# Performance work log

Measured on AMD Instinct MI355X. Metric: run time of the kernel, lower is better.

Reference implementation:

```python
import jax, jax.numpy as jnp
import numpy as np
import math

# normalizer: the module takes it as a callable; we use a standard smooth
# inverse-norm normalizer 1/sqrt(x^2 + eps) applied to the e_inf-like component.
_EPS = 1e-3

def _normalizer(x):
    return 1.0 / jnp.sqrt(x * x + _EPS)


def _dist_vec(tri, basis):
    # tri: (B,H,N,C,5); basis: (5,5,6)
    # vec[...,z] = sum_{x,y} basis[x,y,z] * tri_n[...,x] * tri_n[...,y]
    tri_n = tri * _normalizer(tri[..., 4:5])
    return jnp.einsum('xyz,bhncx,bhncy->bhncz', basis, tri_n, tri_n)


def setup_inputs() -> dict:
    key = jax.random.key(0)
    ks = jax.random.split(key, 8)
    B, H, N, C, S = 1, 8, 4096, 8, 16
    return {
        'q_mv': jax.random.normal(ks[0], (B, H, N, C, 32), jnp.float32),
        'k_mv': jax.random.normal(ks[1], (B, H, N, C, 32), jnp.float32),
        'v_mv': jax.random.normal(ks[2], (B, H, N, C, 32), jnp.float32),
        'q_s': jax.random.normal(ks[3], (B, H, N, S), jnp.float32),
        'k_s': jax.random.normal(ks[4], (B, H, N, S), jnp.float32),
        'v_s': jax.random.normal(ks[5], (B, H, N, S), jnp.float32),
        'basis_q': jax.random.normal(ks[6], (5, 5, 6), jnp.float32),
        'basis_k': jax.random.normal(ks[7], (5, 5, 6), jnp.float32),
    }


def reference(q_mv, k_mv, v_mv, q_s, k_s, v_s, basis_q, basis_k):
    B, H, N, C_qk, _ = q_mv.shape
    C_v = v_mv.shape[-2]
    S_qk = q_s.shape[-1]
    S_v = v_s.shape[-1]
    NUM_IP = 30   # len(_INNER_PRODUCT_WO_EXTREMES_IDX) = indices 1..30
    NUM_DIST = 6
    n_qk = C_qk * (NUM_IP + NUM_DIST) + S_qk
    n_v = C_v * 32 + S_v
    n_ch = 8 * (-(-max(n_qk, n_v) // 8))  # round up to multiple of 8

    # grade-1 components -> distance features
    q_dist = _dist_vec(q_mv[..., 1:6], basis_q)  # (B,H,N,C,6)
    k_dist = _dist_vec(k_mv[..., 1:6], basis_k)

    # inner-product components (indices 1..30)
    q_ip = q_mv[..., 1:31].reshape(B, H, N, C_qk * NUM_IP)
    k_ip = k_mv[..., 1:31].reshape(B, H, N, C_qk * NUM_IP)

    zpad_qk = jnp.zeros((B, H, N, n_ch - n_qk), q_mv.dtype)
    zpad_v = jnp.zeros((B, H, N, n_ch - n_v), v_mv.dtype)

    q = jnp.concatenate([q_ip, q_dist.reshape(B, H, N, -1), q_s, zpad_qk], -1)
    k = jnp.concatenate([k_ip, k_dist.reshape(B, H, N, -1), k_s, zpad_qk], -1)
    v = jnp.concatenate([v_mv.reshape(B, H, N, C_v * 32), v_s, zpad_v], -1)
    k = k * math.sqrt(n_ch / n_qk)

    # standard scaled dot-product attention with scale 1/sqrt(n_ch)
    scale = 1.0 / math.sqrt(n_ch)
    scores = jnp.einsum('bhqd,bhkd->bhqk', q, k) * scale
    attn = jax.nn.softmax(scores, axis=-1)
    v_out = jnp.einsum('bhqk,bhkd->bhqd', attn, v)

    v_out_mv = v_out[..., :C_v * 32].reshape(B, H, N, C_v, 32)
    v_out_s = v_out[..., C_v * 32:C_v * 32 + S_v]
    return (v_out_mv, v_out_s)
```

## Files before the change

### kernel.cpp

```cpp
#include <hip/hip_runtime.h>
#include <math.h>

typedef short bf16x8 __attribute__((ext_vector_type(8)));
typedef float f32x4 __attribute__((ext_vector_type(4)));
typedef int   i32x4 __attribute__((ext_vector_type(4)));

#define HH 8
#define NN 4096
#define DIP 256
#define DDX 256
#define DKM 192
#define DV 272
#define BN 32
#define NT (NN/BN)

typedef const __attribute__((address_space(1))) unsigned int* gp_t;
typedef __attribute__((address_space(3))) unsigned int* lp_t;
__device__ __forceinline__ void gload16(const void* g, void* l) {
    __builtin_amdgcn_global_load_lds((gp_t)g, (lp_t)l, 16, 0, 0);
}

__device__ __forceinline__ unsigned short f2bf(float f) {
    unsigned int u = __float_as_uint(f);
    u = (u + 0x7fffu + ((u >> 16) & 1u)) >> 16;
    return (unsigned short)u;
}
__device__ __forceinline__ float bf2f(unsigned short h) {
    return __uint_as_float(((unsigned int)h) << 16);
}
__device__ __forceinline__ float fexp2(float x) {
    float r;
    asm("v_exp_f32 %0, %1" : "=v"(r) : "v"(x));
    return r;
}
__device__ __forceinline__ signed char q8(float x) {
    int v = __float2int_rn(x * 21.1666667f);
    v = v < -127 ? -127 : (v > 127 ? 127 : v);
    return (signed char)v;
}

#define MFMA16(A,B,C) __builtin_amdgcn_mfma_f32_16x16x32_bf16((A),(B),(C),0,0,0)
#define MFMAI8(A,B,C) __builtin_amdgcn_mfma_i32_16x16x64_i8((A),(B),(C),0,0,0)

__global__ void feat_kernel(const float* __restrict__ mv,
                            const float* __restrict__ sv,
                            const float* __restrict__ basis,
                            float scale, int qmode,
                            signed char* __restrict__ fip,
                            unsigned short* __restrict__ fdx)
{
    __shared__ float sb[150];
    int t = threadIdx.x;
    if (t < 150) sb[t] = basis[t];
    __syncthreads();
    int row = blockIdx.x * 32 + (t >> 3);
    int c = t & 7;
    const float* m = mv + (size_t)row * 256 + c * 32;
    float f[32];
    #pragma unroll
    for (int i = 0; i < 8; ++i) {
        float4 v = ((const float4*)m)[i];
        f[i*4+0] = v.x; f[i*4+1] = v.y; f[i*4+2] = v.z; f[i*4+3] = v.w;
    }
    signed char* ip = fip + (size_t)row * DIP;
    unsigned short* dx = fdx + (size_t)row * (qmode ? DDX : DKM);
    #pragma unroll
    for (int j = 0; j < 30; ++j)
        ip[c*30 + j] = q8(f[1+j]);
    if (c < 2) {
        #pragma unroll
        for (int i = 0; i < 8; ++i)
            ip[240 + c*8 + i] = q8(sv[(size_t)row*16 + c*8 + i]);
    }
    float nn = 1.0f / sqrtf(f[5]*f[5] + 0.001f);
    float tn[5];
    #pragma unroll
    for (int x = 0; x < 5; ++x) tn[x] = f[1+x] * nn;
    #pragma unroll
    for (int z = 0; z < 6; ++z) {
        float acc = 0.f;
        #pragma unroll
        for (int x = 0; x < 5; ++x) {
            #pragma unroll
            for (int y = 0; y < 5; ++y)
                acc = fmaf(sb[(x*5+y)*6 + z] * tn[x], tn[y], acc);
        }
        acc *= scale;
        unsigned short hi = f2bf(acc);
        float r1 = acc - bf2f(hi);
        unsigned short mi = f2bf(r1);
        float r2 = r1 - bf2f(mi);
        unsigned short lo = f2bf(r2);
        int cz = c*6 + z;
        if (qmode) {
            dx[cz]      = hi;  dx[48 + cz]  = hi;
            dx[96 + cz] = mi;  dx[144 + cz] = lo;
            if (cz < 16) { dx[208 + cz] = 0; dx[240 + cz] = 0; }
            if (cz >= 32) { dx[160 + cz] = mi; dx[192 + cz] = hi; }
        } else {
            dx[cz]      = mi;  dx[48 + cz]  = lo;
            dx[96 + cz] = hi;  dx[144 + cz] = hi;
        }
    }
}

__global__ void vtrans_kernel(const float* __restrict__ vmv,
                              const float* __restrict__ vs,
                              unsigned short* __restrict__ dst)
{
    __shared__ unsigned short tile[64][DV];
    int blk = blockIdx.x;
    int h = blk >> 6;
    int n0 = (blk & 63) << 6;
    int t = threadIdx.x;
    #pragma unroll
    for (int it = 0; it < 16; ++it) {
        int v = t + it*256;
        int r = v >> 6;
        int sg = v & 63;
        float4 x = *(const float4*)(vmv + ((size_t)(h*NN + n0 + r))*256 + sg*4);
        tile[r][sg*4+0] = f2bf(x.x);
        tile[r][sg*4+1] = f2bf(x.y);
        tile[r][sg*4+2] = f2bf(x.z);
        tile[r][sg*4+3] = f2bf(x.w);
    }
    #pragma unroll
    for (int it = 0; it < 4; ++it) {
        int v = t + it*256;
        int r = v >> 4;
        int si = v & 15;
        tile[r][256 + si] = f2bf(vs[((size_t)(h*NN + n0 + r))*16 + si]);
    }
    __syncthreads();
    #pragma unroll
    for (int it = 0; it < 17; ++it) {
        int v = t + it*256;
        int dd = v >> 4;
        int sg = v & 15;
        ushort4 o;
        o.x = tile[sg*4+0][dd];
        o.y = tile[sg*4+1][dd];
        o.z = tile[sg*4+2][dd];
        o.w = tile[sg*4+3][dd];
        *(ushort4*)(dst + ((size_t)(h*DV + dd))*NN + n0 + sg*4) = o;
    }
}

__global__ __launch_bounds__(512, 1)
void attn_kernel(const signed char*    __restrict__ Qip,
                 const unsigned short* __restrict__ Qdx,
                 const signed char*    __restrict__ Kip,
                 const unsigned short* __restrict__ Kmx,
                 const unsigned short* __restrict__ Vt,
                 float* __restrict__ out)
{
    __shared__ __align__(128) unsigned short smem[41984];

    int blk = blockIdx.x;
    int sbk = ((blk & 7) << 5) | (blk >> 3);
    int h = sbk >> 5;
    int q0 = (sbk & 31) * 128;
    int tid = threadIdx.x;
    int w = tid >> 6;
    int lane = tid & 63;
    int l15 = lane & 15;
    int l4 = lane >> 4;
    int l7l = l15 & 3;
    int l7h = (l15 >> 2) & 1;
    int x7 = l15 & 7;

    const signed char* qipr = Qip + (size_t)(h*NN + q0 + w*16 + l15) * DIP + l4*16;
    i32x4 qip[4];
    #pragma unroll
    for (int s = 0; s < 4; ++s) qip[s] = *(const i32x4*)(qipr + s*64);
    const unsigned short* qdxr = Qdx + (size_t)(h*NN + q0 + w*16 + l15) * DDX + l4*8;
    bf16x8 qdx[8];
    #pragma unroll
    for (int ks = 0; ks < 8; ++ks) qdx[ks] = *(const bf16x8*)(qdxr + ks*32);

    int cl16 = (l4 ^ l7l) * 16;
    int mA  = l15*384 + cl16 + l7h*64;
    int mB  = l15*384 + cl16 + 64 - l7h*64;
    int vlane = (l15>>1)*128 + (((((l15&1)<<2) | l4) ^ (l15>>1)) << 4);
    int pbR = 75776 + w*1024 + l15*64;
    int pSeg0 = pbR + ((((l4>>1)    ) ^ l7l) << 4) + (l4&1)*8;
    int pSeg1 = pbR + ((((l4>>1) + 2) ^ l7l) << 4) + (l4&1)*8;
    int pRd   = pbR + ((l4 ^ l7l) << 4);
    int kti[4];
    #pragma unroll
    for (int s = 0; s < 4; ++s)
        kti[s] = l15*256 + (((s*4 + l4) ^ x7) << 4);

    int kt8s;
    { int r_ = tid >> 4, sg_ = tid & 15;
      kt8s = r_*256 + ((sg_ ^ (r_ & 7)) << 4); }
    int km0s, km1vt, vt1s, vt2s;
#define KMFL(SLOT, DST) { int r_ = (SLOT)/24, fp_ = (SLOT)%24; \
    int g_ = fp_>>3, po_ = fp_&7; \
    int pl_ = ((((po_>>2)&1) ^ ((r_>>2)&1)) << 2) | ((po_&3) ^ (r_&3)); \
    DST = r_*DKM + (g_*8 + pl_)*8; }
#define VTF(SLOT, DST) { int ch_ = (SLOT) >> 3, ws_ = (SLOT) & 7; int lw_ = ws_ ^ (ch_&7); \
    DST = (ch_*2 + (lw_>>2))*NN + (lw_&3)*8; }
    KMFL(tid, km0s)
    if (tid < 256) { KMFL(tid+512, km1vt) } else { VTF(tid-256, km1vt) }
    VTF(tid+256, vt1s)
    VTF(tid+768, vt2s)
#undef KMFL
#undef VTF

    const signed char*    kiph = Kip + (size_t)h*NN*DIP;
    const unsigned short* kmxh = Kmx + (size_t)h*NN*DKM;
    const unsigned short* vh   = Vt  + (size_t)h*DV*NN;

    f32x4 zero = {0.f, 0.f, 0.f, 0.f};
    i32x4 zi = {0, 0, 0, 0};
    f32x4 oacc[17];
    #pragma unroll
    for (int ct = 0; ct < 17; ++ct) oacc[ct] = zero;
    float mreg = -__builtin_inff();
    float lreg = 0.f;
    const float F = 0.08274443827037988f * (6.0f/127.0f) * (6.0f/127.0f);

#define ISSUE(TILE, BUF) do { \
    const signed char* ks_ = kiph + (size_t)(TILE)*BN*DIP; \
    const unsigned short* ms_ = kmxh + (size_t)(TILE)*BN*DKM; \
    const unsigned short* vs_ = vh + (TILE)*BN; \
    char* ktd_ = (char*)smem + (BUF)*8192; \
    unsigned short* kmd_ = smem + 8192 + (BUF)*6144; \
    unsigned short* vtd_ = smem + 20480 + (BUF)*8704; \
    gload16(ks_ + kt8s, ktd_ + tid*16); \
    gload16(ms_ + km0s, kmd_ + tid*8); \
    if (tid < 256) gload16(ms_ + km1vt, kmd_ + (512+tid)*8); \
    else           gload16(vs_ + km1vt, vtd_ + (tid-256)*8); \
    gload16(vs_ + vt1s, vtd_ + (tid+256)*8); \
    if (tid < 320) gload16(vs_ + vt2s, vtd_ + (tid+768)*8); \
} while (0)

    ISSUE(0, 0);
    int cur = 0;
    #pragma unroll 1
    for (int t = 0; t < NT; ++t) {
        if (t < NT-1) ISSUE(t+1, cur^1);
        if (t < NT-1) {
            if (w < 5) asm volatile("s_waitcnt vmcnt(5)" ::: "memory");
            else       asm volatile("s_waitcnt vmcnt(4)" ::: "memory");
        } else {
            asm volatile("s_waitcnt vmcnt(0)" ::: "memory");
        }
        __builtin_amdgcn_sched_barrier(0);
        __builtin_amdgcn_s_barrier();
        __builtin_amdgcn_sched_barrier(0);

        const char* ktb = (const char*)smem + cur*8192;
        const char* kmb = (const char*)smem + 16384 + cur*12288;
        const char* vtb = (const char*)smem + 40960 + cur*17408;
        f32x4 sacc0 = zero, sacc1 = zero;
        i32x4 si0 = zi, si1 = zi;
        __builtin_amdgcn_s_setprio(1);
        #pragma unroll
        for (int s = 0; s < 4; ++s) {
            i32x4 a0 = *(const i32x4*)(ktb + kti[s]);
            i32x4 a1 = *(const i32x4*)(ktb + 4096 + kti[s]);
            si0 = MFMAI8(a0, qip[s], si0);
            si1 = MFMAI8(a1, qip[s], si1);
        }
        #pragma unroll
        for (int ct = 0; ct < 2; ++ct) {
            const char* kk = kmb + ct*6144;
            bf16x8 ka0 = *(const bf16x8*)(kk + mA);
            bf16x8 ka1 = *(const bf16x8*)(kk + mB);
            bf16x8 ka2 = *(const bf16x8*)(kk + mA + 128);
            bf16x8 kb0 = *(const bf16x8*)(kk + mB + 128);
            bf16x8 kb1 = *(const bf16x8*)(kk + mA + 256);
            bf16x8 kb2 = *(const bf16x8*)(kk + mB + 256);
            f32x4 a = (ct == 0) ? sacc0 : sacc1;
            a = MFMA16(ka0, qdx[0], a);
            a = MFMA16(ka1, qdx[1], a);
            a = MFMA16(ka2, qdx[2], a);
            a = MFMA16(kb0, qdx[3], a);
            a = MFMA16(kb1, qdx[4], a);
            a = MFMA16(kb2, qdx[5], a);
            a = MFMA16(ka0, qdx[3], a);
            a = MFMA16(ka1, qdx[6], a);
            a = MFMA16(kb0, qdx[0], a);
            a = MFMA16(kb1, qdx[7], a);
            if (ct == 0) sacc0 = a; else sacc1 = a;
        }
        __builtin_amdgcn_s_setprio(0);
        f32x4 sn0, sn1;
        sn0[0] = sacc0[0] + F * (float)si0[0];
        sn0[1] = sacc0[1] + F * (float)si0[1];
        sn0[2] = sacc0[2] + F * (float)si0[2];
        sn0[3] = sacc0[3] + F * (float)si0[3];
        sn1[0] = sacc1[0] + F * (float)si1[0];
        sn1[1] = sacc1[1] + F * (float)si1[1];
        sn1[2] = sacc1[2] + F * (float)si1[2];
        sn1[3] = sacc1[3] + F * (float)si1[3];

        float pm = fmaxf(fmaxf(fmaxf(sn0[0], sn0[1]), fmaxf(sn0[2], sn0[3])),
                         fmaxf(fmaxf(sn1[0], sn1[1]), fmaxf(sn1[2], sn1[3])));
        pm = fmaxf(pm, __shfl_xor(pm, 16, 64));
        pm = fmaxf(pm, __shfl_xor(pm, 32, 64));
        if (!__all(pm <= mreg + 8.0f)) {
            float mnew = fmaxf(mreg, pm);
            float al = fexp2(mreg - mnew);
            mreg = mnew;
            lreg *= al;
            float a0 = __shfl(al, l4*4+0, 64);
            float a1 = __shfl(al, l4*4+1, 64);
            float a2 = __shfl(al, l4*4+2, 64);
            float a3 = __shfl(al, l4*4+3, 64);
            #pragma unroll
            for (int ct = 0; ct < 17; ++ct) {
                oacc[ct][0] *= a0; oacc[ct][1] *= a1;
                oacc[ct][2] *= a2; oacc[ct][3] *= a3;
            }
        }
        float p0 = fexp2(sn0[0] - mreg), p1 = fexp2(sn0[1] - mreg);
        float p2 = fexp2(sn0[2] - mreg), p3 = fexp2(sn0[3] - mreg);
        float p4 = fexp2(sn1[0] - mreg), p5 = fexp2(sn1[1] - mreg);
        float p6 = fexp2(sn1[2] - mreg), p7 = fexp2(sn1[3] - mreg);
        lreg += ((p0 + p1) + (p2 + p3)) + ((p4 + p5) + (p6 + p7));
        unsigned r01, r23, r45, r67;
        asm("v_cvt_pk_bf16_f32 %0, %1, %2" : "=v"(r01) : "v"(p0), "v"(p1));
        asm("v_cvt_pk_bf16_f32 %0, %1, %2" : "=v"(r23) : "v"(p2), "v"(p3));
        asm("v_cvt_pk_bf16_f32 %0, %1, %2" : "=v"(r45) : "v"(p4), "v"(p5));
        asm("v_cvt_pk_bf16_f32 %0, %1, %2" : "=v"(r67) : "v"(p6), "v"(p7));
        {
            char* pbp = (char*)smem;
            *(unsigned*)(pbp + pSeg0 + 0) = r01;
            *(unsigned*)(pbp + pSeg0 + 4) = r23;
            *(unsigned*)(pbp + pSeg1 + 0) = r45;
            *(unsigned*)(pbp + pSeg1 + 4) = r67;
        }

        {
            bf16x8 pa = *(const bf16x8*)((const char*)smem + pRd);
            __builtin_amdgcn_s_setprio(1);
            #pragma unroll
            for (int ct = 0; ct < 17; ++ct) {
                bf16x8 bv = *(const bf16x8*)(vtb + vlane + ct*1024);
                oacc[ct] = MFMA16(pa, bv, oacc[ct]);
            }
            __builtin_amdgcn_s_setprio(0);
        }
        __builtin_amdgcn_s_barrier();
        __builtin_amdgcn_sched_barrier(0);
        cur ^= 1;
    }
#undef ISSUE

    float lf = lreg;
    lf += __shfl_xor(lf, 16, 64);
    lf += __shfl_xor(lf, 32, 64);
    const size_t mv_total = (size_t)HH * NN * 256;
    #pragma unroll
    for (int j = 0; j < 4; ++j) {
        float inv = 1.0f / __shfl(lf, l4*4 + j, 64);
        int q = q0 + w*16 + l4*4 + j;
        float* po = out + ((size_t)h*NN + q) * 256 + l15;
        #pragma unroll
        for (int ct = 0; ct < 16; ++ct)
            po[ct*16] = oacc[ct][j] * inv;
        out[mv_total + ((size_t)h*NN + q)*16 + l15] = oacc[16][j] * inv;
    }
}

extern "C" void kernel_launch(void* const* d_in, const int* in_sizes, int n_in,
                              void* d_out, int out_size, void* d_ws, size_t ws_size,
                              hipStream_t stream)
{
    const float* q_mv = (const float*)d_in[0];
    const float* k_mv = (const float*)d_in[1];
    const float* v_mv = (const float*)d_in[2];
    const float* q_s  = (const float*)d_in[3];
    const float* k_s  = (const float*)d_in[4];
    const float* v_s  = (const float*)d_in[5];
    const float* basis_q = (const float*)d_in[6];
    const float* basis_k = (const float*)d_in[7];
    float* out = (float*)d_out;

    signed char* qip8 = (signed char*)d_ws;
    signed char* kip8 = qip8 + (size_t)HH*NN*DIP;
    unsigned short* qdx = (unsigned short*)(kip8 + (size_t)HH*NN*DIP);
    unsigned short* kmx = qdx + (size_t)HH*NN*DDX;
    unsigned short* vt  = kmx + (size_t)HH*NN*DKM;

    const float qscale = 0.08274443827037988f;

    feat_kernel<<<dim3(1024), dim3(256), 0, stream>>>(q_mv, q_s, basis_q, qscale, 1, qip8, qdx);
    feat_kernel<<<dim3(1024), dim3(256), 0, stream>>>(k_mv, k_s, basis_k, 1.0f,   0, kip8, kmx);
    vtrans_kernel<<<dim3(512), dim3(256), 0, stream>>>(v_mv, v_s, vt);
    attn_kernel<<<dim3(256), dim3(512), 0, stream>>>(qip8, qdx, kip8, kmx, vt, out);
}
```

Measured before the change: 280.6 us.

## Double KV tile width and split K/V prefetch into separate pipeline stages

Result: faster. 258.2 us (median of 2 runs) (-8.0%).

```diff
diff --git a/kernel.cpp b/kernel.cpp
--- a/kernel.cpp
+++ b/kernel.cpp
@@ -11,7 +11,7 @@
 #define DDX 256
 #define DKM 192
 #define DV 272
-#define BN 32
+#define BN 64
 #define NT (NN/BN)
 
 typedef const __attribute__((address_space(1))) unsigned int* gp_t;
@@ -154,7 +154,7 @@
                  const unsigned short* __restrict__ Vt,
                  float* __restrict__ out)
 {
-    __shared__ __align__(128) unsigned short smem[41984];
+    __shared__ __align__(128) unsigned short smem[66560];
 
     int blk = blockIdx.x;
     int sbk = ((blk & 7) << 5) | (blk >> 3);
@@ -181,31 +181,34 @@
     int cl16 = (l4 ^ l7l) * 16;
     int mA  = l15*384 + cl16 + l7h*64;
     int mB  = l15*384 + cl16 + 64 - l7h*64;
-    int vlane = (l15>>1)*128 + (((((l15&1)<<2) | l4) ^ (l15>>1)) << 4);
-    int pbR = 75776 + w*1024 + l15*64;
-    int pSeg0 = pbR + ((((l4>>1)    ) ^ l7l) << 4) + (l4&1)*8;
-    int pSeg1 = pbR + ((((l4>>1) + 2) ^ l7l) << 4) + (l4&1)*8;
-    int pRd   = pbR + ((l4 ^ l7l) << 4);
     int kti[4];
     #pragma unroll
     for (int s = 0; s < 4; ++s)
         kti[s] = l15*256 + (((s*4 + l4) ^ x7) << 4);
-
-    int kt8s;
-    { int r_ = tid >> 4, sg_ = tid & 15;
-      kt8s = r_*256 + ((sg_ ^ (r_ & 7)) << 4); }
-    int km0s, km1vt, vt1s, vt2s;
+    int vb0 = (l15>>1)*256 + ((((l15&1)*8 + l4) ^ (l15>>1)) << 4);
+    int vb1 = (l15>>1)*256 + ((((l15&1)*8 + 4 + l4) ^ (l15>>1)) << 4);
+    int pbW = 116736 + w*2048 + l15*128;
+    int pw[4];
+    #pragma unroll
+    for (int kt4 = 0; kt4 < 4; ++kt4)
+        pw[kt4] = pbW + (((kt4*2 + (l4>>1)) ^ x7) << 4) + ((l4&1) << 3);
+    int pr0 = pbW + ((l4 ^ x7) << 4);
+    int pr1 = pbW + (((4+l4) ^ x7) << 4);
+
+    int kts0, kts1;
+    { int idx = tid;       int r_ = idx>>4, sg_ = idx&15; kts0 = r_*256 + ((sg_ ^ (r_&7))<<4); }
+    { int idx = tid+512;   int r_ = idx>>4, sg_ = idx&15; kts1 = r_*256 + ((sg_ ^ (r_&7))<<4); }
+    int kms0, kms1, kms2;
 #define KMFL(SLOT, DST) { int r_ = (SLOT)/24, fp_ = (SLOT)%24; \
     int g_ = fp_>>3, po_ = fp_&7; \
     int pl_ = ((((po_>>2)&1) ^ ((r_>>2)&1)) << 2) | ((po_&3) ^ (r_&3)); \
     DST = r_*DKM + (g_*8 + pl_)*8; }
-#define VTF(SLOT, DST) { int ch_ = (SLOT) >> 3, ws_ = (SLOT) & 7; int lw_ = ws_ ^ (ch_&7); \
-    DST = (ch_*2 + (lw_>>2))*NN + (lw_&3)*8; }
-    KMFL(tid, km0s)
-    if (tid < 256) { KMFL(tid+512, km1vt) } else { VTF(tid-256, km1vt) }
-    VTF(tid+256, vt1s)
-    VTF(tid+768, vt2s)
+    KMFL(tid, kms0) KMFL(tid+512, kms1) KMFL(tid+1024, kms2)
 #undef KMFL
+    int vts0, vts1, vts2, vts3, vts4;
+#define VTF(SLOT, DST) { int ch_ = (SLOT)>>4, ps_ = (SLOT)&15; int ls_ = ps_ ^ (ch_&7); \
+    DST = (ch_*2 + (ls_>>3))*NN + (ls_&7)*8; }
+    VTF(tid, vts0) VTF(tid+512, vts1) VTF(tid+1024, vts2) VTF(tid+1536, vts3) VTF(tid+2048, vts4)
 #undef VTF
 
     const signed char*    kiph = Kip + (size_t)h*NN*DIP;
@@ -221,84 +224,96 @@
     float lreg = 0.f;
     const float F = 0.08274443827037988f * (6.0f/127.0f) * (6.0f/127.0f);
 
-#define ISSUE(TILE, BUF) do { \
+#define ISSUE_K(TILE, BUF) do { \
     const signed char* ks_ = kiph + (size_t)(TILE)*BN*DIP; \
     const unsigned short* ms_ = kmxh + (size_t)(TILE)*BN*DKM; \
+    char* ktd_ = (char*)smem + (BUF)*16384; \
+    char* kmd_ = (char*)smem + 32768 + (BUF)*24576; \
+    gload16(ks_ + kts0, ktd_ + tid*16); \
+    gload16(ks_ + kts1, ktd_ + (tid+512)*16); \
+    gload16(ms_ + kms0, kmd_ + tid*16); \
+    gload16(ms_ + kms1, kmd_ + (tid+512)*16); \
+    gload16(ms_ + kms2, kmd_ + (tid+1024)*16); \
+} while (0)
+
+#define ISSUE_V(TILE) do { \
     const unsigned short* vs_ = vh + (TILE)*BN; \
-    char* ktd_ = (char*)smem + (BUF)*8192; \
-    unsigned short* kmd_ = smem + 8192 + (BUF)*6144; \
-    unsigned short* vtd_ = smem + 20480 + (BUF)*8704; \
-    gload16(ks_ + kt8s, ktd_ + tid*16); \
-    gload16(ms_ + km0s, kmd_ + tid*8); \
-    if (tid < 256) gload16(ms_ + km1vt, kmd_ + (512+tid)*8); \
-    else           gload16(vs_ + km1vt, vtd_ + (tid-256)*8); \
-    gload16(vs_ + vt1s, vtd_ + (tid+256)*8); \
-    if (tid < 320) gload16(vs_ + vt2s, vtd_ + (tid+768)*8); \
+    char* vtd_ = (char*)smem + 81920; \
+    gload16(vs_ + vts0, vtd_ + tid*16); \
+    gload16(vs_ + vts1, vtd_ + (tid+512)*16); \
+    gload16(vs_ + vts2, vtd_ + (tid+1024)*16); \
+    gload16(vs_ + vts3, vtd_ + (tid+1536)*16); \
+    if (tid < 128) gload16(vs_ + vts4, vtd_ + (tid+2048)*16); \
 } while (0)
 
-    ISSUE(0, 0);
+    ISSUE_K(0, 0);
     int cur = 0;
     #pragma unroll 1
     for (int t = 0; t < NT; ++t) {
-        if (t < NT-1) ISSUE(t+1, cur^1);
+        ISSUE_V(t);
         if (t < NT-1) {
-            if (w < 5) asm volatile("s_waitcnt vmcnt(5)" ::: "memory");
+            ISSUE_K(t+1, cur^1);
+            if (w < 2) asm volatile("s_waitcnt vmcnt(10)" ::: "memory");
+            else       asm volatile("s_waitcnt vmcnt(9)"  ::: "memory");
+        } else {
+            if (w < 2) asm volatile("s_waitcnt vmcnt(5)" ::: "memory");
             else       asm volatile("s_waitcnt vmcnt(4)" ::: "memory");
-        } else {
-            asm volatile("s_waitcnt vmcnt(0)" ::: "memory");
         }
         __builtin_amdgcn_sched_barrier(0);
         __builtin_amdgcn_s_barrier();
         __builtin_amdgcn_sched_barrier(0);
 
-        const char* ktb = (const char*)smem + cur*8192;
-        const char* kmb = (const char*)smem + 16384 + cur*12288;
-        const char* vtb = (const char*)smem + 40960 + cur*17408;
-        f32x4 sacc0 = zero, sacc1 = zero;
-        i32x4 si0 = zi, si1 = zi;
+        const char* ktb = (const char*)smem + cur*16384;
+        const char* kmb = (const char*)smem + 32768 + cur*24576;
+
+        f32x4 sf[4];
+        i32x4 si[4];
         __builtin_amdgcn_s_setprio(1);
         #pragma unroll
-        for (int s = 0; s < 4; ++s) {
-            i32x4 a0 = *(const i32x4*)(ktb + kti[s]);
-            i32x4 a1 = *(const i32x4*)(ktb + 4096 + kti[s]);
-            si0 = MFMAI8(a0, qip[s], si0);
-            si1 = MFMAI8(a1, qip[s], si1);
-        }
-        #pragma unroll
-        for (int ct = 0; ct < 2; ++ct) {
-            const char* kk = kmb + ct*6144;
+        for (int kt4 = 0; kt4 < 4; ++kt4) {
+            const char* kb = ktb + kt4*4096;
+            i32x4 a = zi;
+            a = MFMAI8(*(const i32x4*)(kb + kti[0]), qip[0], a);
+            a = MFMAI8(*(const i32x4*)(kb + kti[1]), qip[1], a);
+            a = MFMAI8(*(const i32x4*)(kb + kti[2]), qip[2], a);
+            a = MFMAI8(*(const i32x4*)(kb + kti[3]), qip[3], a);
+            si[kt4] = a;
+            const char* kk = kmb + kt4*6144;
             bf16x8 ka0 = *(const bf16x8*)(kk + mA);
             bf16x8 ka1 = *(const bf16x8*)(kk + mB);
             bf16x8 ka2 = *(const bf16x8*)(kk + mA + 128);
             bf16x8 kb0 = *(const bf16x8*)(kk + mB + 128);
             bf16x8 kb1 = *(const bf16x8*)(kk + mA + 256);
             bf16x8 kb2 = *(const bf16x8*)(kk + mB + 256);
-            f32x4 a = (ct == 0) ? sacc0 : sacc1;
-            a = MFMA16(ka0, qdx[0], a);
-            a = MFMA16(ka1, qdx[1], a);
-            a = MFMA16(ka2, qdx[2], a);
-            a = MFMA16(kb0, qdx[3], a);
-            a = MFMA16(kb1, qdx[4], a);
-            a = MFMA16(kb2, qdx[5], a);
-            a = MFMA16(ka0, qdx[3], a);
-            a = MFMA16(ka1, qdx[6], a);
-            a = MFMA16(kb0, qdx[0], a);
-            a = MFMA16(kb1, qdx[7], a);
-            if (ct == 0) sacc0 = a; else sacc1 = a;
+            f32x4 d = zero;
+            d = MFMA16(ka0, qdx[0], d);
+            d = MFMA16(ka1, qdx[1], d);
+            d = MFMA16(ka2, qdx[2], d);
+            d = MFMA16(kb0, qdx[3], d);
+            d = MFMA16(kb1, qdx[4], d);
+            d = MFMA16(kb2, qdx[5], d);
+            d = MFMA16(ka0, qdx[3], d);
+            d = MFMA16(ka1, qdx[6], d);
+            d = MFMA16(kb0, qdx[0], d);
+            d = MFMA16(kb1, qdx[7], d);
+            sf[kt4] = d;
         }
         __builtin_amdgcn_s_setprio(0);
-        f32x4 sn0, sn1;
-        sn0[0] = sacc0[0] + F * (float)si0[0];
-        sn0[1] = sacc0[1] + F * (float)si0[1];
-        sn0[2] = sacc0[2] + F * (float)si0[2];
-        sn0[3] = sacc0[3] + F * (float)si0[3];
-        sn1[0] = sacc1[0] + F * (float)si1[0];
-        sn1[1] = sacc1[1] + F * (float)si1[1];
-        sn1[2] = sacc1[2] + F * (float)si1[2];
-        sn1[3] = sacc1[3] + F * (float)si1[3];
-
-        float pm = fmaxf(fmaxf(fmaxf(sn0[0], sn0[1]), fmaxf(sn0[2], sn0[3])),
-                         fmaxf(fmaxf(sn1[0], sn1[1]), fmaxf(sn1[2], sn1[3])));
+
+        f32x4 sn[4];
+        #pragma unroll
+        for (int kt4 = 0; kt4 < 4; ++kt4) {
+            sn[kt4][0] = sf[kt4][0] + F * (float)si[kt4][0];
+            sn[kt4][1] = sf[kt4][1] + F * (float)si[kt4][1];
+            sn[kt4][2] = sf[kt4][2] + F * (float)si[kt4][2];
+            sn[kt4][3] = sf[kt4][3] + F * (float)si[kt4][3];
+        }
+
+        float pm = fmaxf(
+            fmaxf(fmaxf(fmaxf(sn[0][0], sn[0][1]), fmaxf(sn[0][2], sn[0][3])),
+                  fmaxf(fmaxf(sn[1][0], sn[1][1]), fmaxf(sn[1][2], sn[1][3]))),
+            fmaxf(fmaxf(fmaxf(sn[2][0], sn[2][1]), fmaxf(sn[2][2], sn[2][3])),
+                  fmaxf(fmaxf(sn[3][0], sn[3][1]), fmaxf(sn[3][2], sn[3][3]))));
         pm = fmaxf(pm, __shfl_xor(pm, 16, 64));
         pm = fmaxf(pm, __shfl_xor(pm, 32, 64));
         if (!__all(pm <= mreg + 8.0f)) {
@@ -316,31 +331,39 @@
                 oacc[ct][2] *= a2; oacc[ct][3] *= a3;
             }
         }
-        float p0 = fexp2(sn0[0] - mreg), p1 = fexp2(sn0[1] - mreg);
-        float p2 = fexp2(sn0[2] - mreg), p3 = fexp2(sn0[3] - mreg);
-        float p4 = fexp2(sn1[0] - mreg), p5 = fexp2(sn1[1] - mreg);
-        float p6 = fexp2(sn1[2] - mreg), p7 = fexp2(sn1[3] - mreg);
-        lreg += ((p0 + p1) + (p2 + p3)) + ((p4 + p5) + (p6 + p7));
-        unsigned r01, r23, r45, r67;
-        asm("v_cvt_pk_bf16_f32 %0, %1, %2" : "=v"(r01) : "v"(p0), "v"(p1));
-        asm("v_cvt_pk_bf16_f32 %0, %1, %2" : "=v"(r23) : "v"(p2), "v"(p3));
-        asm("v_cvt_pk_bf16_f32 %0, %1, %2" : "=v"(r45) : "v"(p4), "v"(p5));
-        asm("v_cvt_pk_bf16_f32 %0, %1, %2" : "=v"(r67) : "v"(p6), "v"(p7));
+        char* pbp = (char*)smem;
+        #pragma unroll
+        for (int kt4 = 0; kt4 < 4; ++kt4) {
+            float p0 = fexp2(sn[kt4][0] - mreg), p1 = fexp2(sn[kt4][1] - mreg);
+            float p2 = fexp2(sn[kt4][2] - mreg), p3 = fexp2(sn[kt4][3] - mreg);
+            lreg += (p0 + p1) + (p2 + p3);
+            unsigned r01, r23;
+            asm("v_cvt_pk_bf16_f32 %0, %1, %2" : "=v"(r01) : "v"(p0), "v"(p1));
+            asm("v_cvt_pk_bf16_f32 %0, %1, %2" : "=v"(r23) : "v"(p2), "v"(p3));
+            unsigned long long pk = ((unsigned long long)r23 << 32) | (unsigned long long)r01;
+            *(unsigned long long*)(pbp + pw[kt4]) = pk;
+        }
+
+        if (t < NT-1) asm volatile("s_waitcnt vmcnt(5)" ::: "memory");
+        else          asm volatile("s_waitcnt vmcnt(0)" ::: "memory");
+        __builtin_amdgcn_sched_barrier(0);
+        __builtin_amdgcn_s_barrier();
+        __builtin_amdgcn_sched_barrier(0);
+
         {
-            char* pbp = (char*)smem;
-            *(unsigned*)(pbp + pSeg0 + 0) = r01;
-            *(unsigned*)(pbp + pSeg0 + 4) = r23;
-            *(unsigned*)(pbp + pSeg1 + 0) = r45;
-            *(unsigned*)(pbp + pSeg1 + 4) = r67;
-        }
-
-        {
-            bf16x8 pa = *(const bf16x8*)((const char*)smem + pRd);
+            bf16x8 pa0 = *(const bf16x8*)(pbp + pr0);
+            bf16x8 pa1 = *(const bf16x8*)(pbp + pr1);
+            const char* vtb = (const char*)smem + 81920;
             __builtin_amdgcn_s_setprio(1);
             #pragma unroll
             for (int ct = 0; ct < 17; ++ct) {
-                bf16x8 bv = *(const bf16x8*)(vtb + vlane + ct*1024);
-                oacc[ct] = MFMA16(pa, bv, oacc[ct]);
+                bf16x8 bv0 = *(const bf16x8*)(vtb + ct*2048 + vb0);
+                oacc[ct] = MFMA16(pa0, bv0, oacc[ct]);
+            }
+            #pragma unroll
+            for (int ct = 0; ct < 17; ++ct) {
+                bf16x8 bv1 = *(const bf16x8*)(vtb + ct*2048 + vb1);
+                oacc[ct] = MFMA16(pa1, bv1, oacc[ct]);
             }
             __builtin_amdgcn_s_setprio(0);
         }
@@ -348,7 +371,8 @@
         __builtin_amdgcn_sched_barrier(0);
         cur ^= 1;
     }
-#undef ISSUE
+#undef ISSUE_K
+#undef ISSUE_V
 
     float lf = lreg;
     lf += __shfl_xor(lf, 16, 64);
```

## Process two query tiles per wave and single-buffer V with split barrier

Applied to the files above, without the earlier changes.

Measured after the change: 722.0 us. 2.57x slower.

```diff
diff --git a/kernel.cpp b/kernel.cpp
--- a/kernel.cpp
+++ b/kernel.cpp
@@ -146,7 +146,7 @@
     }
 }
 
-__global__ __launch_bounds__(512, 1)
+__global__ __launch_bounds__(256, 2)
 void attn_kernel(const signed char*    __restrict__ Qip,
                  const unsigned short* __restrict__ Qdx,
                  const signed char*    __restrict__ Kip,
@@ -154,7 +154,7 @@
                  const unsigned short* __restrict__ Vt,
                  float* __restrict__ out)
 {
-    __shared__ __align__(128) unsigned short smem[41984];
+    __shared__ __align__(128) unsigned short smem[33280];
 
     int blk = blockIdx.x;
     int sbk = ((blk & 7) << 5) | (blk >> 3);
@@ -169,43 +169,48 @@
     int l7h = (l15 >> 2) & 1;
     int x7 = l15 & 7;
 
-    const signed char* qipr = Qip + (size_t)(h*NN + q0 + w*16 + l15) * DIP + l4*16;
-    i32x4 qip[4];
-    #pragma unroll
-    for (int s = 0; s < 4; ++s) qip[s] = *(const i32x4*)(qipr + s*64);
-    const unsigned short* qdxr = Qdx + (size_t)(h*NN + q0 + w*16 + l15) * DDX + l4*8;
-    bf16x8 qdx[8];
-    #pragma unroll
-    for (int ks = 0; ks < 8; ++ks) qdx[ks] = *(const bf16x8*)(qdxr + ks*32);
+    const signed char* qipr = Qip + (size_t)(h*NN + q0 + w*32 + l15) * DIP + l4*16;
+    i32x4 qip[4][2];
+    #pragma unroll
+    for (int s = 0; s < 4; ++s) {
+        qip[s][0] = *(const i32x4*)(qipr + s*64);
+        qip[s][1] = *(const i32x4*)(qipr + 16*DIP + s*64);
+    }
+    const unsigned short* qdxr = Qdx + (size_t)(h*NN + q0 + w*32 + l15) * DDX + l4*8;
+    bf16x8 qdx[8][2];
+    #pragma unroll
+    for (int ks = 0; ks < 8; ++ks) {
+        qdx[ks][0] = *(const bf16x8*)(qdxr + ks*32);
+        qdx[ks][1] = *(const bf16x8*)(qdxr + 16*DDX + ks*32);
+    }
 
     int cl16 = (l4 ^ l7l) * 16;
     int mA  = l15*384 + cl16 + l7h*64;
     int mB  = l15*384 + cl16 + 64 - l7h*64;
-    int vlane = (l15>>1)*128 + (((((l15&1)<<2) | l4) ^ (l15>>1)) << 4);
-    int pbR = 75776 + w*1024 + l15*64;
-    int pSeg0 = pbR + ((((l4>>1)    ) ^ l7l) << 4) + (l4&1)*8;
-    int pSeg1 = pbR + ((((l4>>1) + 2) ^ l7l) << 4) + (l4&1)*8;
-    int pRd   = pbR + ((l4 ^ l7l) << 4);
     int kti[4];
     #pragma unroll
     for (int s = 0; s < 4; ++s)
         kti[s] = l15*256 + (((s*4 + l4) ^ x7) << 4);
-
-    int kt8s;
-    { int r_ = tid >> 4, sg_ = tid & 15;
-      kt8s = r_*256 + ((sg_ ^ (r_ & 7)) << 4); }
-    int km0s, km1vt, vt1s, vt2s;
+    int vlane = (l15>>1)*128 + (((((l15&1)<<2) | l4) ^ (l15>>1)) << 4);
+    int pbW = 58368 + w*2048 + l15*64;
+    int pSeg0 = pbW + ((((l4>>1)    ) ^ l7l) << 4) + (l4&1)*8;
+    int pSeg1 = pbW + ((((l4>>1) + 2) ^ l7l) << 4) + (l4&1)*8;
+    int pRd   = pbW + ((l4 ^ l7l) << 4);
+
+    int kts0, kts1;
+    { int s_ = tid;     int r_ = s_>>4, sg_ = s_&15; kts0 = r_*256 + ((sg_ ^ (r_&7))<<4); }
+    { int s_ = tid+256; int r_ = s_>>4, sg_ = s_&15; kts1 = r_*256 + ((sg_ ^ (r_&7))<<4); }
+    int kms0, kms1, kms2;
 #define KMFL(SLOT, DST) { int r_ = (SLOT)/24, fp_ = (SLOT)%24; \
     int g_ = fp_>>3, po_ = fp_&7; \
     int pl_ = ((((po_>>2)&1) ^ ((r_>>2)&1)) << 2) | ((po_&3) ^ (r_&3)); \
     DST = r_*DKM + (g_*8 + pl_)*8; }
+    KMFL(tid, kms0) KMFL(tid+256, kms1) KMFL(tid+512, kms2)
+#undef KMFL
+    int vts0, vts1, vts2, vts3, vts4;
 #define VTF(SLOT, DST) { int ch_ = (SLOT) >> 3, ws_ = (SLOT) & 7; int lw_ = ws_ ^ (ch_&7); \
     DST = (ch_*2 + (lw_>>2))*NN + (lw_&3)*8; }
-    KMFL(tid, km0s)
-    if (tid < 256) { KMFL(tid+512, km1vt) } else { VTF(tid-256, km1vt) }
-    VTF(tid+256, vt1s)
-    VTF(tid+768, vt2s)
-#undef KMFL
+    VTF(tid, vts0) VTF(tid+256, vts1) VTF(tid+512, vts2) VTF(tid+768, vts3) VTF(tid+1024, vts4)
 #undef VTF
 
     const signed char*    kiph = Kip + (size_t)h*NN*DIP;
@@ -214,38 +219,47 @@
 
     f32x4 zero = {0.f, 0.f, 0.f, 0.f};
     i32x4 zi = {0, 0, 0, 0};
-    f32x4 oacc[17];
-    #pragma unroll
-    for (int ct = 0; ct < 17; ++ct) oacc[ct] = zero;
-    float mreg = -__builtin_inff();
-    float lreg = 0.f;
+    f32x4 oacc[17][2];
+    #pragma unroll
+    for (int ct = 0; ct < 17; ++ct) { oacc[ct][0] = zero; oacc[ct][1] = zero; }
+    float m0 = -__builtin_inff(), l0 = 0.f;
+    float m1 = -__builtin_inff(), l1 = 0.f;
     const float F = 0.08274443827037988f * (6.0f/127.0f) * (6.0f/127.0f);
 
-#define ISSUE(TILE, BUF) do { \
+#define ISSUE_K(TILE, BUF) do { \
     const signed char* ks_ = kiph + (size_t)(TILE)*BN*DIP; \
     const unsigned short* ms_ = kmxh + (size_t)(TILE)*BN*DKM; \
+    char* ktd_ = (char*)smem + (BUF)*8192; \
+    char* kmd_ = (char*)smem + 16384 + (BUF)*12288; \
+    gload16(ks_ + kts0, ktd_ + tid*16); \
+    gload16(ks_ + kts1, ktd_ + (tid+256)*16); \
+    gload16(ms_ + kms0, kmd_ + tid*16); \
+    gload16(ms_ + kms1, kmd_ + (tid+256)*16); \
+    gload16(ms_ + kms2, kmd_ + (tid+512)*16); \
+} while (0)
+
+#define ISSUE_V(TILE) do { \
     const unsigned short* vs_ = vh + (TILE)*BN; \
-    char* ktd_ = (char*)smem + (BUF)*8192; \
-    unsigned short* kmd_ = smem + 8192 + (BUF)*6144; \
-    unsigned short* vtd_ = smem + 20480 + (BUF)*8704; \
-    gload16(ks_ + kt8s, ktd_ + tid*16); \
-    gload16(ms_ + km0s, kmd_ + tid*8); \
-    if (tid < 256) gload16(ms_ + km1vt, kmd_ + (512+tid)*8); \
-    else           gload16(vs_ + km1vt, vtd_ + (tid-256)*8); \
-    gload16(vs_ + vt1s, vtd_ + (tid+256)*8); \
-    if (tid < 320) gload16(vs_ + vt2s, vtd_ + (tid+768)*8); \
+    char* vtd_ = (char*)smem + 40960; \
+    gload16(vs_ + vts0, vtd_ + tid*16); \
+    gload16(vs_ + vts1, vtd_ + (tid+256)*16); \
+    gload16(vs_ + vts2, vtd_ + (tid+512)*16); \
+    gload16(vs_ + vts3, vtd_ + (tid+768)*16); \
+    if (tid < 64) gload16(vs_ + vts4, vtd_ + (tid+1024)*16); \
 } while (0)
 
-    ISSUE(0, 0);
+    ISSUE_K(0, 0);
     int cur = 0;
     #pragma unroll 1
     for (int t = 0; t < NT; ++t) {
-        if (t < NT-1) ISSUE(t+1, cur^1);
+        ISSUE_V(t);
         if (t < NT-1) {
-            if (w < 5) asm volatile("s_waitcnt vmcnt(5)" ::: "memory");
-            else       asm volatile("s_waitcnt vmcnt(4)" ::: "memory");
+            ISSUE_K(t+1, cur^1);
+            if (w == 0) asm volatile("s_waitcnt vmcnt(10)" ::: "memory");
+            else        asm volatile("s_waitcnt vmcnt(9)"  ::: "memory");
         } else {
-            asm volatile("s_waitcnt vmcnt(0)" ::: "memory");
+            if (w == 0) asm volatile("s_waitcnt vmcnt(5)" ::: "memory");
+            else        asm volatile("s_waitcnt vmcnt(4)" ::: "memory");
         }
         __builtin_amdgcn_sched_barrier(0);
         __builtin_amdgcn_s_barrier();
@@ -253,94 +267,139 @@
 
         const char* ktb = (const char*)smem + cur*8192;
         const char* kmb = (const char*)smem + 16384 + cur*12288;
-        const char* vtb = (const char*)smem + 40960 + cur*17408;
-        f32x4 sacc0 = zero, sacc1 = zero;
-        i32x4 si0 = zi, si1 = zi;
+
+        i32x4 si00 = zi, si01 = zi, si10 = zi, si11 = zi;
         __builtin_amdgcn_s_setprio(1);
         #pragma unroll
         for (int s = 0; s < 4; ++s) {
             i32x4 a0 = *(const i32x4*)(ktb + kti[s]);
             i32x4 a1 = *(const i32x4*)(ktb + 4096 + kti[s]);
-            si0 = MFMAI8(a0, qip[s], si0);
-            si1 = MFMAI8(a1, qip[s], si1);
-        }
+            si00 = MFMAI8(a0, qip[s][0], si00);
+            si01 = MFMAI8(a0, qip[s][1], si01);
+            si10 = MFMAI8(a1, qip[s][0], si10);
+            si11 = MFMAI8(a1, qip[s][1], si11);
+        }
+        f32x4 sn00, sn01, sn10, sn11;
         #pragma unroll
-        for (int ct = 0; ct < 2; ++ct) {
-            const char* kk = kmb + ct*6144;
+        for (int j = 0; j < 4; ++j) {
+            sn00[j] = F * (float)si00[j];
+            sn01[j] = F * (float)si01[j];
+            sn10[j] = F * (float)si10[j];
+            sn11[j] = F * (float)si11[j];
+        }
+        {
+            const char* kk = kmb;
             bf16x8 ka0 = *(const bf16x8*)(kk + mA);
             bf16x8 ka1 = *(const bf16x8*)(kk + mB);
             bf16x8 ka2 = *(const bf16x8*)(kk + mA + 128);
             bf16x8 kb0 = *(const bf16x8*)(kk + mB + 128);
             bf16x8 kb1 = *(const bf16x8*)(kk + mA + 256);
             bf16x8 kb2 = *(const bf16x8*)(kk + mB + 256);
-            f32x4 a = (ct == 0) ? sacc0 : sacc1;
-            a = MFMA16(ka0, qdx[0], a);
-            a = MFMA16(ka1, qdx[1], a);
-            a = MFMA16(ka2, qdx[2], a);
-            a = MFMA16(kb0, qdx[3], a);
-            a = MFMA16(kb1, qdx[4], a);
-            a = MFMA16(kb2, qdx[5], a);
-            a = MFMA16(ka0, qdx[3], a);
-            a = MFMA16(ka1, qdx[6], a);
-            a = MFMA16(kb0, qdx[0], a);
-            a = MFMA16(kb1, qdx[7], a);
-            if (ct == 0) sacc0 = a; else sacc1 = a;
+            sn00 = MFMA16(ka0, qdx[0][0], sn00);  sn01 = MFMA16(ka0, qdx[0][1], sn01);
+            sn00 = MFMA16(ka1, qdx[1][0], sn00);  sn01 = MFMA16(ka1, qdx[1][1], sn01);
+            sn00 = MFMA16(ka2, qdx[2][0], sn00);  sn01 = MFMA16(ka2, qdx[2][1], sn01);
+            sn00 = MFMA16(kb0, qdx[3][0], sn00);  sn01 = MFMA16(kb0, qdx[3][1], sn01);
+            sn00 = MFMA16(kb1, qdx[4][0], sn00);  sn01 = MFMA16(kb1, qdx[4][1], sn01);
+            sn00 = MFMA16(kb2, qdx[5][0], sn00);  sn01 = MFMA16(kb2, qdx[5][1], sn01);
+            sn00 = MFMA16(ka0, qdx[3][0], sn00);  sn01 = MFMA16(ka0, qdx[3][1], sn01);
+            sn00 = MFMA16(ka1, qdx[6][0], sn00);  sn01 = MFMA16(ka1, qdx[6][1], sn01);
+            sn00 = MFMA16(kb0, qdx[0][0], sn00);  sn01 = MFMA16(kb0, qdx[0][1], sn01);
+            sn00 = MFMA16(kb1, qdx[7][0], sn00);  sn01 = MFMA16(kb1, qdx[7][1], sn01);
+        }
+        {
+            const char* kk = kmb + 6144;
+            bf16x8 ka0 = *(const bf16x8*)(kk + mA);
+            bf16x8 ka1 = *(const bf16x8*)(kk + mB);
+            bf16x8 ka2 = *(const bf16x8*)(kk + mA + 128);
+            bf16x8 kb0 = *(const bf16x8*)(kk + mB + 128);
+            bf16x8 kb1 = *(const bf16x8*)(kk + mA + 256);
+            bf16x8 kb2 = *(const bf16x8*)(kk + mB + 256);
+            sn10 = MFMA16(ka0, qdx[0][0], sn10);  sn11 = MFMA16(ka0, qdx[0][1], sn11);
+            sn10 = MFMA16(ka1, qdx[1][0], sn10);  sn11 = MFMA16(ka1, qdx[1][1], sn11);
+            sn10 = MFMA16(ka2, qdx[2][0], sn10);  sn11 = MFMA16(ka2, qdx[2][1], sn11);
+            sn10 = MFMA16(kb0, qdx[3][0], sn10);  sn11 = MFMA16(kb0, qdx[3][1], sn11);
+            sn10 = MFMA16(kb1, qdx[4][0], sn10);  sn11 = MFMA16(kb1, qdx[4][1], sn11);
+            sn10 = MFMA16(kb2, qdx[5][0], sn10);  sn11 = MFMA16(kb2, qdx[5][1], sn11);
+            sn10 = MFMA16(ka0, qdx[3][0], sn10);  sn11 = MFMA16(ka0, qdx[3][1], sn11);
+            sn10 = MFMA16(ka1, qdx[6][0], sn10);  sn11 = MFMA16(ka1, qdx[6][1], sn11);
+            sn10 = MFMA16(kb0, qdx[0][0], sn10);  sn11 = MFMA16(kb0, qdx[0][1], sn11);
+            sn10 = MFMA16(kb1, qdx[7][0], sn10);  sn11 = MFMA16(kb1, qdx[7][1], sn11);
         }
         __builtin_amdgcn_s_setprio(0);
-        f32x4 sn0, sn1;
-        sn0[0] = sacc0[0] + F * (float)si0[0];
-        sn0[1] = sacc0[1] + F * (float)si0[1];
-        sn0[2] = sacc0[2] + F * (float)si0[2];
-        sn0[3] = sacc0[3] + F * (float)si0[3];
-        sn1[0] = sacc1[0] + F * (float)si1[0];
-        sn1[1] = sacc1[1] + F * (float)si1[1];
-        sn1[2] = sacc1[2] + F * (float)si1[2];
-        sn1[3] = sacc1[3] + F * (float)si1[3];
-
-        float pm = fmaxf(fmaxf(fmaxf(sn0[0], sn0[1]), fmaxf(sn0[2], sn0[3])),
-                         fmaxf(fmaxf(sn1[0], sn1[1]), fmaxf(sn1[2], sn1[3])));
-        pm = fmaxf(pm, __shfl_xor(pm, 16, 64));
-        pm = fmaxf(pm, __shfl_xor(pm, 32, 64));
-        if (!__all(pm <= mreg + 8.0f)) {
-            float mnew = fmaxf(mreg, pm);
-            float al = fexp2(mreg - mnew);
-            mreg = mnew;
-            lreg *= al;
-            float a0 = __shfl(al, l4*4+0, 64);
-            float a1 = __shfl(al, l4*4+1, 64);
-            float a2 = __shfl(al, l4*4+2, 64);
-            float a3 = __shfl(al, l4*4+3, 64);
+
+        float pm0 = fmaxf(fmaxf(fmaxf(sn00[0], sn00[1]), fmaxf(sn00[2], sn00[3])),
+                          fmaxf(fmaxf(sn10[0], sn10[1]), fmaxf(sn10[2], sn10[3])));
+        float pm1 = fmaxf(fmaxf(fmaxf(sn01[0], sn01[1]), fmaxf(sn01[2], sn01[3])),
+                          fmaxf(fmaxf(sn11[0], sn11[1]), fmaxf(sn11[2], sn11[3])));
+        pm0 = fmaxf(pm0, __shfl_xor(pm0, 16, 64));
+        pm0 = fmaxf(pm0, __shfl_xor(pm0, 32, 64));
+        pm1 = fmaxf(pm1, __shfl_xor(pm1, 16, 64));
+        pm1 = fmaxf(pm1, __shfl_xor(pm1, 32, 64));
+        bool ok0 = __all(pm0 <= m0 + 8.0f);
+        bool ok1 = __all(pm1 <= m1 + 8.0f);
+        if (!(ok0 && ok1)) {
+            float mn0 = fmaxf(m0, pm0), mn1 = fmaxf(m1, pm1);
+            float al0 = fexp2(m0 - mn0), al1 = fexp2(m1 - mn1);
+            m0 = mn0; m1 = mn1;
+            l0 *= al0; l1 *= al1;
+            float a00 = __shfl(al0, l4*4+0, 64), a01 = __shfl(al0, l4*4+1, 64);
+            float a02 = __shfl(al0, l4*4+2, 64), a03 = __shfl(al0, l4*4+3, 64);
+            float a10 = __shfl(al1, l4*4+0, 64), a11 = __shfl(al1, l4*4+1, 64);
+            float a12 = __shfl(al1, l4*4+2, 64), a13 = __shfl(al1, l4*4+3, 64);
             #pragma unroll
             for (int ct = 0; ct < 17; ++ct) {
-                oacc[ct][0] *= a0; oacc[ct][1] *= a1;
-                oacc[ct][2] *= a2; oacc[ct][3] *= a3;
+                oacc[ct][0][0] *= a00; oacc[ct][0][1] *= a01;
+                oacc[ct][0][2] *= a02; oacc[ct][0][3] *= a03;
+                oacc[ct][1][0] *= a10; oacc[ct][1][1] *= a11;
+                oacc[ct][1][2] *= a12; oacc[ct][1][3] *= a13;
             }
         }
-        float p0 = fexp2(sn0[0] - mreg), p1 = fexp2(sn0[1] - mreg);
-        float p2 = fexp2(sn0[2] - mreg), p3 = fexp2(sn0[3] - mreg);
-        float p4 = fexp2(sn1[0] - mreg), p5 = fexp2(sn1[1] - mreg);
-        float p6 = fexp2(sn1[2] - mreg), p7 = fexp2(sn1[3] - mreg);
-        lreg += ((p0 + p1) + (p2 + p3)) + ((p4 + p5) + (p6 + p7));
-        unsigned r01, r23, r45, r67;
-        asm("v_cvt_pk_bf16_f32 %0, %1, %2" : "=v"(r01) : "v"(p0), "v"(p1));
-        asm("v_cvt_pk_bf16_f32 %0, %1, %2" : "=v"(r23) : "v"(p2), "v"(p3));
-        asm("v_cvt_pk_bf16_f32 %0, %1, %2" : "=v"(r45) : "v"(p4), "v"(p5));
-        asm("v_cvt_pk_bf16_f32 %0, %1, %2" : "=v"(r67) : "v"(p6), "v"(p7));
+        char* pbp = (char*)smem;
         {
-            char* pbp = (char*)smem;
-            *(unsigned*)(pbp + pSeg0 + 0) = r01;
-            *(unsigned*)(pbp + pSeg0 + 4) = r23;
-            *(unsigned*)(pbp + pSeg1 + 0) = r45;
-            *(unsigned*)(pbp + pSeg1 + 4) = r67;
-        }
-
+            float p0 = fexp2(sn00[0] - m0), p1 = fexp2(sn00[1] - m0);
+            float p2 = fexp2(sn00[2] - m0), p3 = fexp2(sn00[3] - m0);
+            float p4 = fexp2(sn10[0] - m0), p5 = fexp2(sn10[1] - m0);
+            float p6 = fexp2(sn10[2] - m0), p7 = fexp2(sn10[3] - m0);
+            l0 += ((p0 + p1) + (p2 + p3)) + ((p4 + p5) + (p6 + p7));
+            unsigned r01, r23, r45, r67;
+            asm("v_cvt_pk_bf16_f32 %0, %1, %2" : "=v"(r01) : "v"(p0), "v"(p1));
+            asm("v_cvt_pk_bf16_f32 %0, %1, %2" : "=v"(r23) : "v"(p2), "v"(p3));
+            asm("v_cvt_pk_bf16_f32 %0, %1, %2" : "=v"(r45) : "v"(p4), "v"(p5));
+            asm("v_cvt_pk_bf16_f32 %0, %1, %2" : "=v"(r67) : "v"(p6), "v"(p7));
+            *(unsigned long long*)(pbp + pSeg0) = ((unsigned long long)r23 << 32) | r01;
+            *(unsigned long long*)(pbp + pSeg1) = ((unsigned long long)r67 << 32) | r45;
+        }
         {
-            bf16x8 pa = *(const bf16x8*)((const char*)smem + pRd);
+            float p0 = fexp2(sn01[0] - m1), p1 = fexp2(sn01[1] - m1);
+            float p2 = fexp2(sn01[2] - m1), p3 = fexp2(sn01[3] - m1);
+            float p4 = fexp2(sn11[0] - m1), p5 = fexp2(sn11[1] - m1);
+            float p6 = fexp2(sn11[2] - m1), p7 = fexp2(sn11[3] - m1);
+            l1 += ((p0 + p1) + (p2 + p3)) + ((p4 + p5) + (p6 + p7));
+            unsigned r01, r23, r45, r67;
+            asm("v_cvt_pk_bf16_f32 %0, %1, %2" : "=v"(r01) : "v"(p0), "v"(p1));
+            asm("v_cvt_pk_bf16_f32 %0, %1, %2" : "=v"(r23) : "v"(p2), "v"(p3));
+            asm("v_cvt_pk_bf16_f32 %0, %1, %2" : "=v"(r45) : "v"(p4), "v"(p5));
+            asm("v_cvt_pk_bf16_f32 %0, %1, %2" : "=v"(r67) : "v"(p6), "v"(p7));
+            *(unsigned long long*)(pbp + pSeg0 + 1024) = ((unsigned long long)r23 << 32) | r01;
+            *(unsigned long long*)(pbp + pSeg1 + 1024) = ((unsigned long long)r67 << 32) | r45;
+        }
+
+        if (t < NT-1) asm volatile("s_waitcnt vmcnt(5)" ::: "memory");
+        else          asm volatile("s_waitcnt vmcnt(0)" ::: "memory");
+        __builtin_amdgcn_sched_barrier(0);
+        __builtin_amdgcn_s_barrier();
+        __builtin_amdgcn_sched_barrier(0);
+
+        {
+            bf16x8 pa0 = *(const bf16x8*)(pbp + pRd);
+            bf16x8 pa1 = *(const bf16x8*)(pbp + pRd + 1024);
+            const char* vtb = (const char*)smem + 40960;
             __builtin_amdgcn_s_setprio(1);
             #pragma unroll
             for (int ct = 0; ct < 17; ++ct) {
                 bf16x8 bv = *(const bf16x8*)(vtb + vlane + ct*1024);
-                oacc[ct] = MFMA16(pa, bv, oacc[ct]);
+                oacc[ct][0] = MFMA16(pa0, bv, oacc[ct][0]);
+                oacc[ct][1] = MFMA16(pa1, bv, oacc[ct][1]);
             }
             __builtin_amdgcn_s_setprio(0);
         }
@@ -348,21 +407,30 @@
         __builtin_amdgcn_sched_barrier(0);
         cur ^= 1;
     }
-#undef ISSUE
-
-    float lf = lreg;
-    lf += __shfl_xor(lf, 16, 64);
-    lf += __shfl_xor(lf, 32, 64);
+#undef ISSUE_K
+#undef ISSUE_V
+
+    float lf0 = l0, lf1 = l1;
+    lf0 += __shfl_xor(lf0, 16, 64);
+    lf0 += __shfl_xor(lf0, 32, 64);
+    lf1 += __shfl_xor(lf1, 16, 64);
+    lf1 += __shfl_xor(lf1, 32, 64);
     const size_t mv_total = (size_t)HH * NN * 256;
     #pragma unroll
     for (int j = 0; j < 4; ++j) {
-        float inv = 1.0f / __shfl(lf, l4*4 + j, 64);
-        int q = q0 + w*16 + l4*4 + j;
-        float* po = out + ((size_t)h*NN + q) * 256 + l15;
+        float inv0 = 1.0f / __shfl(lf0, l4*4 + j, 64);
+        float inv1 = 1.0f / __shfl(lf1, l4*4 + j, 64);
+        int qA = q0 + w*32 + l4*4 + j;
+        int qB = qA + 16;
+        float* poA = out + ((size_t)h*NN + qA) * 256 + l15;
+        float* poB = out + ((size_t)h*NN + qB) * 256 + l15;
         #pragma unroll
-        for (int ct = 0; ct < 16; ++ct)
-            po[ct*16] = oacc[ct][j] * inv;
-        out[mv_total + ((size_t)h*NN + q)*16 + l15] = oacc[16][j] * inv;
+        for (int ct = 0; ct < 16; ++ct) {
+            poA[ct*16] = oacc[ct][0][j] * inv0;
+            poB[ct*16] = oacc[ct][1][j] * inv1;
+        }
+        out[mv_total + ((size_t)h*NN + qA)*16 + l15] = oacc[16][0][j] * inv0;
+        out[mv_total + ((size_t)h*NN + qB)*16 + l15] = oacc[16][1][j] * inv1;
     }
 }
 
@@ -391,5 +459,5 @@
     feat_kernel<<<dim3(1024), dim3(256), 0, stream>>>(q_mv, q_s, basis_q, qscale, 1, qip8, qdx);
     feat_kernel<<<dim3(1024), dim3(256), 0, stream>>>(k_mv, k_s, basis_k, 1.0f,   0, kip8, kmx);
     vtrans_kernel<<<dim3(512), dim3(256), 0, stream>>>(v_mv, v_s, vt);
-    attn_kernel<<<dim3(256), dim3(512), 0, stream>>>(qip8, qdx, kip8, kmx, vt, out);
-}
+    attn_kernel<<<dim3(256), dim3(256), 0, stream>>>(qip8, qdx, kip8, kmx, vt, out);
+}
```
